# Performance work log

Measured on AMD Instinct MI355X. Metric: run time of the kernel, lower is better.

The kernel has to match this reference:

```python
import jax, jax.numpy as jnp
import numpy as np

N_HEADS = 8
D_KV = 64
NUM_BUCKETS = 32
MAX_DISTANCE = 128


def _relative_position_bucket(relative_position, bidirectional=True,
                              num_buckets=NUM_BUCKETS, max_distance=MAX_DISTANCE):
    # Faithful port of T5Attention._relative_position_bucket (bidirectional path).
    n = -relative_position
    if bidirectional:
        num_buckets //= 2
        ret = (n < 0).astype(jnp.int32) * num_buckets
        n = jnp.abs(n)
    else:
        ret = jnp.zeros_like(n)
        n = jnp.maximum(n, 0)
    max_exact = num_buckets // 2
    is_small = n < max_exact
    val_if_large = max_exact + (
        jnp.log(n.astype(jnp.float32) / max_exact)
        / np.log(max_distance / max_exact)
        * (num_buckets - max_exact)
    ).astype(jnp.int32)
    val_if_large = jnp.minimum(val_if_large, num_buckets - 1)
    return ret + jnp.where(is_small, n, val_if_large)


def setup_inputs() -> dict:
    key = jax.random.key(0)
    ks = jax.random.split(key, 6)
    bs, qlen, d_model = 2, 2048, 512
    inner = N_HEADS * D_KV
    s = 1.0 / np.sqrt(d_model)
    return {
        "input": jax.random.normal(ks[0], (bs, qlen, d_model), jnp.float32),
        "Wq": jax.random.normal(ks[1], (d_model, inner), jnp.float32) * s,
        "Wk": jax.random.normal(ks[2], (d_model, inner), jnp.float32) * s,
        "Wv": jax.random.normal(ks[3], (d_model, inner), jnp.float32) * s,
        "Wo": jax.random.normal(ks[4], (inner, d_model), jnp.float32) * s,
        "rel_bias": jax.random.normal(ks[5], (NUM_BUCKETS, N_HEADS), jnp.float32),
    }


def reference(input, Wq, Wk, Wv, Wo, rel_bias):
    bs, qlen, d_model = input.shape

    def shape(x):  # [b, s, inner] -> [b, h, s, d]
        return x.reshape(bs, qlen, N_HEADS, D_KV).transpose(0, 2, 1, 3)

    q = shape(input @ Wq)
    k = shape(input @ Wk)
    v = shape(input @ Wv)

    # Raw scores (T5: no 1/sqrt(d) scaling)
    scores = jnp.einsum("bhqd,bhkd->bhqk", q, k)

    # Relative position bias: bucket [q, k] -> [h, q, k]
    pos = jnp.arange(qlen)
    rel_pos = pos[None, :] - pos[:, None]  # memory - query
    buckets = _relative_position_bucket(rel_pos, bidirectional=True)
    position_bias = rel_bias[buckets].transpose(2, 0, 1)[None]  # [1, h, q, k]

    scores = scores + position_bias
    weights = jax.nn.softmax(scores.astype(jnp.float32), axis=-1).astype(scores.dtype)

    context = jnp.einsum("bhqk,bhkd->bhqd", weights, v)
    context = context.transpose(0, 2, 1, 3).reshape(bs, qlen, N_HEADS * D_KV)
    return context @ Wo
```

## Files before the change

### kernel.cpp

```cpp
#include <hip/hip_runtime.h>
#include <hip/hip_bf16.h>
#include <cmath>

typedef __bf16 bf16_t;
typedef __bf16 bf16x8 __attribute__((ext_vector_type(8)));
typedef __bf16 bf16x4 __attribute__((ext_vector_type(4)));
typedef float f32x4 __attribute__((ext_vector_type(4)));

#define QLEN 2048
#define DMODEL 512
#define NH 8
#define DKV 64
#define INNER 512
#define LOG2E 1.44269504f
#define THR_LOG2 11.5415603f

__global__ __launch_bounds__(256) void cvt_split(const float* __restrict__ in,
                                                 bf16_t* __restrict__ hi,
                                                 bf16_t* __restrict__ lo, int n4) {
  int i = blockIdx.x * 256 + threadIdx.x;
  if (i >= n4) return;
  float4 v = reinterpret_cast<const float4*>(in)[i];
  bf16x4 h, l;
  #pragma unroll
  for (int j = 0; j < 4; ++j) {
    float x = (&v.x)[j];
    bf16_t hb = (bf16_t)x;
    h[j] = hb;
    l[j] = (bf16_t)(x - (float)hb);
  }
  reinterpret_cast<bf16x4*>(hi)[i] = h;
  reinterpret_cast<bf16x4*>(lo)[i] = l;
}

__global__ __launch_bounds__(256) void transpose512_split_all(
    const float* __restrict__ W0, const float* __restrict__ W1,
    const float* __restrict__ W2, const float* __restrict__ W3,
    bf16_t* __restrict__ H0, bf16_t* __restrict__ L0,
    bf16_t* __restrict__ H1, bf16_t* __restrict__ L1,
    bf16_t* __restrict__ H2, bf16_t* __restrict__ L2,
    bf16_t* __restrict__ H3, bf16_t* __restrict__ L3) {
  __shared__ float tile[32][33];
  int z = blockIdx.z;
  const float* W = z == 0 ? W0 : z == 1 ? W1 : z == 2 ? W2 : W3;
  bf16_t* Whi    = z == 0 ? H0 : z == 1 ? H1 : z == 2 ? H2 : H3;
  bf16_t* Wlo    = z == 0 ? L0 : z == 1 ? L1 : z == 2 ? L2 : L3;
  int bk = blockIdx.x * 32, bn = blockIdx.y * 32;
  int tx = threadIdx.x, ty = threadIdx.y;
  #pragma unroll
  for (int i = 0; i < 32; i += 8)
    tile[ty + i][tx] = W[(size_t)(bk + ty + i) * DMODEL + bn + tx];
  __syncthreads();
  #pragma unroll
  for (int i = 0; i < 32; i += 8) {
    float v = tile[tx][ty + i];
    bf16_t hb = (bf16_t)v;
    size_t o = (size_t)(bn + ty + i) * DMODEL + bk + tx;
    Whi[o] = hb;
    Wlo[o] = (bf16_t)(v - (float)hb);
  }
}

template<int MODE>
__global__ __launch_bounds__(256) void gemm64(const bf16_t* __restrict__ A,
                                              const bf16_t* __restrict__ Bt,
                                              bf16_t* __restrict__ Cb,
                                              float* __restrict__ Cf) {
  __shared__ bf16_t sA[64 * 72];
  __shared__ bf16_t sB[64 * 72];
  const int m0 = blockIdx.x * 64, n0 = blockIdx.y * 64;
  const int tid = threadIdx.x;
  const int lane = tid & 63, w = tid >> 6;
  const int wr = (w >> 1) * 32, wc = (w & 1) * 32;
  const int l16 = lane & 15, lg = lane >> 4;

  f32x4 acc[2][2] = {};

  for (int k0 = 0; k0 < DMODEL; k0 += 64) {
    #pragma unroll
    for (int i = 0; i < 2; ++i) {
      int chunk = tid + i * 256;
      int row = chunk >> 3, c8 = (chunk & 7) * 8;
      *reinterpret_cast<bf16x8*>(&sA[row * 72 + c8]) =
          *reinterpret_cast<const bf16x8*>(&A[(size_t)(m0 + row) * DMODEL + k0 + c8]);
      *reinterpret_cast<bf16x8*>(&sB[row * 72 + c8]) =
          *reinterpret_cast<const bf16x8*>(&Bt[(size_t)(n0 + row) * DMODEL + k0 + c8]);
    }
    __syncthreads();
    #pragma unroll
    for (int ks = 0; ks < 2; ++ks) {
      bf16x8 af[2], bfr[2];
      #pragma unroll
      for (int i = 0; i < 2; ++i)
        af[i] = *reinterpret_cast<const bf16x8*>(&sA[(wr + i * 16 + l16) * 72 + ks * 32 + lg * 8]);
      #pragma unroll
      for (int j = 0; j < 2; ++j)
        bfr[j] = *reinterpret_cast<const bf16x8*>(&sB[(wc + j * 16 + l16) * 72 + ks * 32 + lg * 8]);
      #pragma unroll
      for (int i = 0; i < 2; ++i)
        #pragma unroll
        for (int j = 0; j < 2; ++j)
          acc[i][j] = __builtin_amdgcn_mfma_f32_16x16x32_bf16(af[i], bfr[j], acc[i][j], 0, 0, 0);
    }
    __syncthreads();
  }

  #pragma unroll
  for (int i = 0; i < 2; ++i)
    #pragma unroll
    for (int j = 0; j < 2; ++j)
      #pragma unroll
      for (int r = 0; r < 4; ++r) {
        int m = m0 + wr + i * 16 + lg * 4 + r;
        int n = n0 + wc + j * 16 + l16;
        float v = acc[i][j][r];
        if (MODE == 1) {
          int b = m >> 11, s = m & (QLEN - 1);
          Cb[(size_t)(b * INNER + n) * QLEN + s] = (bf16_t)v;
        } else {
          Cf[(size_t)m * DMODEL + n] = v;
        }
      }
}

__global__ __launch_bounds__(256) void gemm_qk_split(const bf16_t* __restrict__ Ah,
                                                     const bf16_t* __restrict__ Al,
                                                     const bf16_t* __restrict__ Bqh,
                                                     const bf16_t* __restrict__ Bql,
                                                     const bf16_t* __restrict__ Bkh,
                                                     const bf16_t* __restrict__ Bkl,
                                                     bf16_t* __restrict__ Qh,
                                                     bf16_t* __restrict__ Ql,
                                                     bf16_t* __restrict__ Kh,
                                                     bf16_t* __restrict__ Kl) {
  __shared__ bf16_t sAh[64 * 72];
  __shared__ bf16_t sAl[64 * 72];
  __shared__ bf16_t sBh[128 * 72];
  __shared__ bf16_t sBl[128 * 72];
  const int m0 = blockIdx.x * 64;
  const int n0g = blockIdx.y * 128;
  const bool isK = n0g >= 512;
  const int n0 = n0g & 511;
  const bf16_t* __restrict__ Bh = isK ? Bkh : Bqh;
  const bf16_t* __restrict__ Bl = isK ? Bkl : Bql;
  bf16_t* __restrict__ Ch = isK ? Kh : Qh;
  bf16_t* __restrict__ Cl = isK ? Kl : Ql;

  const int tid = threadIdx.x;
  const int lane = tid & 63, w = tid >> 6;
  const int wr = (w >> 1) * 32, wc = (w & 1) * 64;
  const int l16 = lane & 15, lg = lane >> 4;

  f32x4 acc[2][4] = {};

  for (int k0 = 0; k0 < DMODEL; k0 += 64) {
    #pragma unroll
    for (int i = 0; i < 2; ++i) {
      int chunk = tid + i * 256;
      int row = chunk >> 3, c8 = (chunk & 7) * 8;
      size_t ga = (size_t)(m0 + row) * DMODEL + k0 + c8;
      *reinterpret_cast<bf16x8*>(&sAh[row * 72 + c8]) = *reinterpret_cast<const bf16x8*>(&Ah[ga]);
      *reinterpret_cast<bf16x8*>(&sAl[row * 72 + c8]) = *reinterpret_cast<const bf16x8*>(&Al[ga]);
    }
    #pragma unroll
    for (int i = 0; i < 4; ++i) {
      int chunk = tid + i * 256;
      int row = chunk >> 3, c8 = (chunk & 7) * 8;
      size_t gb = (size_t)(n0 + row) * DMODEL + k0 + c8;
      *reinterpret_cast<bf16x8*>(&sBh[row * 72 + c8]) = *reinterpret_cast<const bf16x8*>(&Bh[gb]);
      *reinterpret_cast<bf16x8*>(&sBl[row * 72 + c8]) = *reinterpret_cast<const bf16x8*>(&Bl[gb]);
    }
    __syncthreads();
    #pragma unroll
    for (int ks = 0; ks < 2; ++ks) {
      bf16x8 ah[2], al[2], bh[4], bl[4];
      #pragma unroll
      for (int i = 0; i < 2; ++i) {
        int ro = (wr + i * 16 + l16) * 72 + ks * 32 + lg * 8;
        ah[i] = *reinterpret_cast<const bf16x8*>(&sAh[ro]);
        al[i] = *reinterpret_cast<const bf16x8*>(&sAl[ro]);
      }
      #pragma unroll
      for (int j = 0; j < 4; ++j) {
        int ro = (wc + j * 16 + l16) * 72 + ks * 32 + lg * 8;
        bh[j] = *reinterpret_cast<const bf16x8*>(&sBh[ro]);
        bl[j] = *reinterpret_cast<const bf16x8*>(&sBl[ro]);
      }
      #pragma unroll
      for (int i = 0; i < 2; ++i)
        #pragma unroll
        for (int j = 0; j < 4; ++j) {
          acc[i][j] = __builtin_amdgcn_mfma_f32_16x16x32_bf16(ah[i], bh[j], acc[i][j], 0, 0, 0);
          acc[i][j] = __builtin_amdgcn_mfma_f32_16x16x32_bf16(ah[i], bl[j], acc[i][j], 0, 0, 0);
          acc[i][j] = __builtin_amdgcn_mfma_f32_16x16x32_bf16(al[i], bh[j], acc[i][j], 0, 0, 0);
        }
    }
    __syncthreads();
  }

  #pragma unroll
  for (int i = 0; i < 2; ++i)
    #pragma unroll
    for (int j = 0; j < 4; ++j)
      #pragma unroll
      for (int r = 0; r < 4; ++r) {
        int m = m0 + wr + i * 16 + lg * 4 + r;
        int n = n0 + wc + j * 16 + l16;
        float v = acc[i][j][r];
        if (!isK) v *= LOG2E;
        bf16_t hb = (bf16_t)v;
        size_t o = (size_t)m * INNER + n;
        Ch[o] = hb;
        if (!isK) Cl[o] = (bf16_t)(v - (float)hb);
      }
}

__device__ __forceinline__ float redmax16(float v) {
  v = fmaxf(v, __shfl_xor(v, 1));
  v = fmaxf(v, __shfl_xor(v, 2));
  v = fmaxf(v, __shfl_xor(v, 4));
  v = fmaxf(v, __shfl_xor(v, 8));
  return v;
}
__device__ __forceinline__ float redsum16(float v) {
  v += __shfl_xor(v, 1);
  v += __shfl_xor(v, 2);
  v += __shfl_xor(v, 4);
  v += __shfl_xor(v, 8);
  return v;
}
__device__ __forceinline__ int t5_bucket_abs(int n) {
  if (n < 8)  return n;
  if (n < 12) return 8;
  if (n < 16) return 9;
  if (n < 23) return 10;
  if (n < 32) return 11;
  if (n < 46) return 12;
  if (n < 64) return 13;
  if (n < 91) return 14;
  return 15;
}

#define SPS 68
#define SVS 136

struct StageRegs { bf16x8 kh[2], v[2]; };

__device__ __forceinline__ void stage_load(StageRegs& r, const bf16_t* __restrict__ Kh,
                                           const bf16_t* __restrict__ Vt,
                                           int b, int h, int k0, int tid) {
  #pragma unroll
  for (int i = 0; i < 2; ++i) {
    int chunk = tid + i * 512;
    int krow = chunk >> 3, kc8 = (chunk & 7) * 8;
    int vrow = chunk >> 4, vc8 = (chunk & 15) * 8;
    r.kh[i] = *reinterpret_cast<const bf16x8*>(
        &Kh[(size_t)(b * QLEN + k0 + krow) * INNER + h * DKV + kc8]);
    r.v[i] = *reinterpret_cast<const bf16x8*>(
        &Vt[(size_t)((b * NH + h) * DKV + vrow) * QLEN + k0 + vc8]);
  }
}
__device__ __forceinline__ void stage_write(const StageRegs& r, bf16_t* dKh, bf16_t* dV,
                                            int tid) {
  #pragma unroll
  for (int i = 0; i < 2; ++i) {
    int chunk = tid + i * 512;
    int krow = chunk >> 3, kc8 = (chunk & 7) * 8;
    int vrow = chunk >> 4, vc8 = (chunk & 15) * 8;
    *reinterpret_cast<bf16x8*>(&dKh[krow * 72 + kc8]) = r.kh[i];
    *reinterpret_cast<bf16x8*>(&dV [vrow * SVS + vc8]) = r.v[i];
  }
}

__global__ __launch_bounds__(512, 4) void attn_kernel(const bf16_t* __restrict__ Qh,
                                                      const bf16_t* __restrict__ Ql,
                                                      const bf16_t* __restrict__ Kh,
                                                      const bf16_t* __restrict__ Vt,
                                                      const float* __restrict__ relb,
                                                      bf16_t* __restrict__ ctx) {
  __shared__ bf16_t sKh[128 * 72];
  __shared__ bf16_t sV [64 * SVS];
  __shared__ bf16_t sP [2][64 * SPS];
  __shared__ float sM[2][64], sL[2][64];
  __shared__ float sBiasH[32];
  float* sAcc = (float*)&sP[0][0];

  const int id = blockIdx.x;
  const int lin = (id & 7) * 64 + (id >> 3);
  const int qt = lin & 31, h = (lin >> 5) & 7, b = lin >> 8;

  const int tid = threadIdx.x, lane = tid & 63, w = tid >> 6;
  const int l16 = lane & 15, lg = lane >> 4;
  const int q0 = qt * 64;
  const int qg = w & 3, half = w >> 2;
  const int wq = qg * 16;
  const int kh0 = half * 64;

  if (tid < 32) sBiasH[tid] = relb[tid * NH + h] * LOG2E;

  bf16x8 qh[2], ql[2];
  #pragma unroll
  for (int ks = 0; ks < 2; ++ks) {
    size_t o = (size_t)(b * QLEN + q0 + wq + l16) * INNER + h * DKV + ks * 32 + lg * 8;
    qh[ks] = *reinterpret_cast<const bf16x8*>(&Qh[o]);
    ql[ks] = *reinterpret_cast<const bf16x8*>(&Ql[o]);
  }

  f32x4 acc[4] = {};
  float mrow[4], lpart[4];
  #pragma unroll
  for (int r = 0; r < 4; ++r) { mrow[r] = -INFINITY; lpart[r] = 0.f; }

  const int NT = QLEN / 128;
  StageRegs sreg;
  stage_load(sreg, Kh, Vt, b, h, 0, tid);
  stage_write(sreg, sKh, sV, tid);
  __syncthreads();

  for (int kt = 0; kt < NT; ++kt) {
    const int k0 = kt * 128;
    const bool pf = (kt + 1 < NT);
    if (pf) stage_load(sreg, Kh, Vt, b, h, k0 + 128, tid);

    f32x4 s[4] = {};
    __builtin_amdgcn_s_setprio(1);
    #pragma unroll
    for (int ks = 0; ks < 2; ++ks) {
      bf16x8 kf[4];
      #pragma unroll
      for (int ni = 0; ni < 4; ++ni)
        kf[ni] = *reinterpret_cast<const bf16x8*>(
            &sKh[(kh0 + ni * 16 + l16) * 72 + ks * 32 + lg * 8]);
      #pragma unroll
      for (int ni = 0; ni < 4; ++ni) {
        s[ni] = __builtin_amdgcn_mfma_f32_16x16x32_bf16(qh[ks], kf[ni], s[ni], 0, 0, 0);
        s[ni] = __builtin_amdgcn_mfma_f32_16x16x32_bf16(ql[ks], kf[ni], s[ni], 0, 0, 0);
      }
    }
    __builtin_amdgcn_s_setprio(0);

    const int kbase = k0 + kh0;
    const int dmin = q0 - (kbase + 63);
    const int dmax = q0 + 63 - kbase;
    const bool farP = dmin >= 91, farN = dmax <= -91;
    float fbias = 0.f;
    if (farP) fbias = sBiasH[15];
    else if (farN) fbias = sBiasH[31];
    else {
      #pragma unroll
      for (int ni = 0; ni < 4; ++ni) {
        int kcol = kbase + ni * 16 + l16;
        #pragma unroll
        for (int r = 0; r < 4; ++r) {
          int qrow = q0 + wq + lg * 4 + r;
          int d = qrow - kcol;
          int n = d < 0 ? -d : d;
          int bk = t5_bucket_abs(n) + (d < 0 ? 16 : 0);
          s[ni][r] += sBiasH[bk];
        }
      }
    }

    float c[4], tmx[4];
    #pragma unroll
    for (int r = 0; r < 4; ++r) {
      tmx[r] = fmaxf(fmaxf(s[0][r], s[1][r]), fmaxf(s[2][r], s[3][r]));
      c[r] = mrow[r] - fbias;
    }
    float u = fmaxf(fmaxf(tmx[0] - c[0], tmx[1] - c[1]), fmaxf(tmx[2] - c[2], tmx[3] - c[3]));
    if (__any(u > THR_LOG2)) {
      #pragma unroll
      for (int r = 0; r < 4; ++r) {
        float rm = redmax16(tmx[r]) + fbias;
        float mnew = fmaxf(mrow[r], rm);
        float alpha = exp2f(mrow[r] - mnew);
        mrow[r] = mnew;
        c[r] = mnew - fbias;
        lpart[r] *= alpha;
        #pragma unroll
        for (int di = 0; di < 4; ++di) acc[di][r] *= alpha;
      }
    }

    #pragma unroll
    for (int r = 0; r < 4; ++r) {
      float ps = 0.f;
      #pragma unroll
      for (int ni = 0; ni < 4; ++ni) {
        float p = exp2f(s[ni][r] - c[r]);
        ps += p;
        sP[half][(wq + lg * 4 + r) * SPS + ni * 16 + l16] = (bf16_t)p;
      }
      lpart[r] += ps;
    }

    __builtin_amdgcn_s_setprio(1);
    #pragma unroll
    for (int ks = 0; ks < 2; ++ks) {
      bf16x8 pfr, vf[4];
      pfr = *reinterpret_cast<const bf16x8*>(&sP[half][(wq + l16) * SPS + ks * 32 + lg * 8]);
      #pragma unroll
      for (int di = 0; di < 4; ++di)
        vf[di] = *reinterpret_cast<const bf16x8*>(
            &sV[(di * 16 + l16) * SVS + kh0 + ks * 32 + lg * 8]);
      #pragma unroll
      for (int di = 0; di < 4; ++di)
        acc[di] = __builtin_amdgcn_mfma_f32_16x16x32_bf16(pfr, vf[di], acc[di], 0, 0, 0);
    }
    __builtin_amdgcn_s_setprio(0);

    __syncthreads();
    if (pf) stage_write(sreg, sKh, sV, tid);
    __syncthreads();
  }

  float lrow[4];
  #pragma unroll
  for (int r = 0; r < 4; ++r) lrow[r] = redsum16(lpart[r]);

  if (l16 == 0) {
    #pragma unroll
    for (int r = 0; r < 4; ++r) {
      int row = wq + lg * 4 + r;
      sM[half][row] = mrow[r];
      sL[half][row] = lrow[r];
    }
  }
  __syncthreads();

  float eh[4], denom[4];
  #pragma unroll
  for (int r = 0; r < 4; ++r) {
    int row = wq + lg * 4 + r;
    float m0 = sM[0][row], m1 = sM[1][row];
    float l0 = sL[0][row], l1 = sL[1][row];
    float M = fmaxf(m0, m1);
    float e0 = exp2f(m0 - M), e1 = exp2f(m1 - M);
    denom[r] = l0 * e0 + l1 * e1;
    eh[r] = half ? e1 : e0;
  }

  if (half == 1) {
    #pragma unroll
    for (int di = 0; di < 4; ++di)
      #pragma unroll
      for (int r = 0; r < 4; ++r)
        sAcc[(wq + lg * 4 + r) * SPS + di * 16 + l16] = acc[di][r] * eh[r];
  }
  __syncthreads();

  if (half == 0) {
    #pragma unroll
    for (int di = 0; di < 4; ++di)
      #pragma unroll
      for (int r = 0; r < 4; ++r) {
        int row = wq + lg * 4 + r;
        float v = (acc[di][r] * eh[r] + sAcc[row * SPS + di * 16 + l16]) / denom[r];
        ctx[(size_t)(b * QLEN + q0 + row) * INNER + h * DKV + di * 16 + l16] = (bf16_t)v;
      }
  }
}

extern "C" void kernel_launch(void* const* d_in, const int* in_sizes, int n_in,
                              void* d_out, int out_size, void* d_ws, size_t ws_size,
                              hipStream_t stream) {
  const float* X    = (const float*)d_in[0];
  const float* Wq   = (const float*)d_in[1];
  const float* Wk   = (const float*)d_in[2];
  const float* Wv   = (const float*)d_in[3];
  const float* Wo   = (const float*)d_in[4];
  const float* relb = (const float*)d_in[5];
  float* out = (float*)d_out;

  const size_t WSZ = 262144, XSZ = 2097152;
  bf16_t* ws   = (bf16_t*)d_ws;
  bf16_t* Wq_h = ws;              bf16_t* Wq_l = Wq_h + WSZ;
  bf16_t* Wk_h = Wq_l + WSZ;      bf16_t* Wk_l = Wk_h + WSZ;
  bf16_t* Wv_h = Wk_l + WSZ;      bf16_t* Wv_l = Wv_h + WSZ;
  bf16_t* Wo_h = Wv_l + WSZ;      bf16_t* Wo_l = Wo_h + WSZ;
  bf16_t* Xh   = Wo_l + WSZ;      bf16_t* Xl   = Xh + XSZ;
  bf16_t* Q_h  = Xl + XSZ;        bf16_t* Q_l  = Q_h + XSZ;
  bf16_t* K_h  = Q_l + XSZ;       bf16_t* K_l  = K_h + XSZ;
  bf16_t* Vt   = Xl;
  bf16_t* ctx  = Xh;

  transpose512_split_all<<<dim3(16, 16, 4), dim3(32, 8), 0, stream>>>(
      Wq, Wk, Wv, Wo, Wq_h, Wq_l, Wk_h, Wk_l, Wv_h, Wv_l, Wo_h, Wo_l);

  int n4 = (2 * QLEN * DMODEL) / 4;
  cvt_split<<<n4 / 256, 256, 0, stream>>>(X, Xh, Xl, n4);

  gemm_qk_split<<<dim3(64, 8), 256, 0, stream>>>(Xh, Xl, Wq_h, Wq_l, Wk_h, Wk_l,
                                                 Q_h, Q_l, K_h, K_l);
  gemm64<1><<<dim3(64, 8), 256, 0, stream>>>(Xh, Wv_h, Vt, nullptr);

  attn_kernel<<<dim3(512), 512, 0, stream>>>(Q_h, Q_l, K_h, Vt, relb, ctx);

  gemm64<2><<<dim3(64, 8), 256, 0, stream>>>(ctx, Wo_h, nullptr, out);
}
```

Before: 109.4 us.

## Split attention over key halves with a merge kernel and direct global K/V loads

The attention kernel now splits the key dimension into two halves, launching twice as many blocks. Each block writes a partial normalized context plus the row max and denominator to scratch space (reusing the output and weight buffers). A new merge kernel combines the two halves into ctx. K and V fragments are now read straight from global memory instead of being staged through shared memory with barriers, which cuts LDS use and allows higher occupancy (launch bounds 512,8). The cost is an extra kernel launch, extra global traffic for partials, and uncoalesced or L2-dependent K/V reads.

```diff
diff --git a/kernel.cpp b/kernel.cpp
--- a/kernel.cpp
+++ b/kernel.cpp
@@ -242,61 +242,33 @@
 }
 
 #define SPS 68
-#define SVS 136
-
-struct StageRegs { bf16x8 kh[2], v[2]; };
-
-__device__ __forceinline__ void stage_load(StageRegs& r, const bf16_t* __restrict__ Kh,
-                                           const bf16_t* __restrict__ Vt,
-                                           int b, int h, int k0, int tid) {
-  #pragma unroll
-  for (int i = 0; i < 2; ++i) {
-    int chunk = tid + i * 512;
-    int krow = chunk >> 3, kc8 = (chunk & 7) * 8;
-    int vrow = chunk >> 4, vc8 = (chunk & 15) * 8;
-    r.kh[i] = *reinterpret_cast<const bf16x8*>(
-        &Kh[(size_t)(b * QLEN + k0 + krow) * INNER + h * DKV + kc8]);
-    r.v[i] = *reinterpret_cast<const bf16x8*>(
-        &Vt[(size_t)((b * NH + h) * DKV + vrow) * QLEN + k0 + vc8]);
-  }
-}
-__device__ __forceinline__ void stage_write(const StageRegs& r, bf16_t* dKh, bf16_t* dV,
-                                            int tid) {
-  #pragma unroll
-  for (int i = 0; i < 2; ++i) {
-    int chunk = tid + i * 512;
-    int krow = chunk >> 3, kc8 = (chunk & 7) * 8;
-    int vrow = chunk >> 4, vc8 = (chunk & 15) * 8;
-    *reinterpret_cast<bf16x8*>(&dKh[krow * 72 + kc8]) = r.kh[i];
-    *reinterpret_cast<bf16x8*>(&dV [vrow * SVS + vc8]) = r.v[i];
-  }
-}
-
-__global__ __launch_bounds__(512, 4) void attn_kernel(const bf16_t* __restrict__ Qh,
+#define HALFELEMS 2097152
+
+__global__ __launch_bounds__(512, 8) void attn_kernel(const bf16_t* __restrict__ Qh,
                                                       const bf16_t* __restrict__ Ql,
                                                       const bf16_t* __restrict__ Kh,
                                                       const bf16_t* __restrict__ Vt,
                                                       const float* __restrict__ relb,
-                                                      bf16_t* __restrict__ ctx) {
-  __shared__ bf16_t sKh[128 * 72];
-  __shared__ bf16_t sV [64 * SVS];
-  __shared__ bf16_t sP [2][64 * SPS];
+                                                      bf16_t* __restrict__ pPart,
+                                                      float* __restrict__ pMl) {
+  __shared__ bf16_t sP[2][64 * SPS];
   __shared__ float sM[2][64], sL[2][64];
   __shared__ float sBiasH[32];
   float* sAcc = (float*)&sP[0][0];
 
   const int id = blockIdx.x;
-  const int lin = (id & 7) * 64 + (id >> 3);
-  const int qt = lin & 31, h = (lin >> 5) & 7, b = lin >> 8;
+  const int lin = (id & 7) * 128 + (id >> 3);
+  const int qt = lin & 31, h = (lin >> 5) & 7, b = (lin >> 8) & 1, sp = lin >> 9;
 
   const int tid = threadIdx.x, lane = tid & 63, w = tid >> 6;
   const int l16 = lane & 15, lg = lane >> 4;
   const int q0 = qt * 64;
   const int qg = w & 3, half = w >> 2;
   const int wq = qg * 16;
-  const int kh0 = half * 64;
+  const int kw0 = sp * 1024 + half * 512;
 
   if (tid < 32) sBiasH[tid] = relb[tid * NH + h] * LOG2E;
+  __syncthreads();
 
   bf16x8 qh[2], ql[2];
   #pragma unroll
@@ -311,16 +283,13 @@
   #pragma unroll
   for (int r = 0; r < 4; ++r) { mrow[r] = -INFINITY; lpart[r] = 0.f; }
 
-  const int NT = QLEN / 128;
-  StageRegs sreg;
-  stage_load(sreg, Kh, Vt, b, h, 0, tid);
-  stage_write(sreg, sKh, sV, tid);
-  __syncthreads();
-
-  for (int kt = 0; kt < NT; ++kt) {
-    const int k0 = kt * 128;
-    const bool pf = (kt + 1 < NT);
-    if (pf) stage_load(sreg, Kh, Vt, b, h, k0 + 128, tid);
+  const size_t kLane = (size_t)l16 * INNER + lg * 8;
+  const size_t vLane = (size_t)l16 * QLEN + lg * 8;
+  size_t kBase = (size_t)(b * QLEN + kw0) * INNER + h * DKV;
+  size_t vBase = (size_t)((b * NH + h) * DKV) * QLEN + kw0;
+
+  for (int it = 0; it < 8; ++it) {
+    const int kbase = kw0 + it * 64;
 
     f32x4 s[4] = {};
     __builtin_amdgcn_s_setprio(1);
@@ -330,7 +299,7 @@
       #pragma unroll
       for (int ni = 0; ni < 4; ++ni)
         kf[ni] = *reinterpret_cast<const bf16x8*>(
-            &sKh[(kh0 + ni * 16 + l16) * 72 + ks * 32 + lg * 8]);
+            &Kh[kBase + (size_t)ni * 16 * INNER + kLane + ks * 32]);
       #pragma unroll
       for (int ni = 0; ni < 4; ++ni) {
         s[ni] = __builtin_amdgcn_mfma_f32_16x16x32_bf16(qh[ks], kf[ni], s[ni], 0, 0, 0);
@@ -339,7 +308,6 @@
     }
     __builtin_amdgcn_s_setprio(0);
 
-    const int kbase = k0 + kh0;
     const int dmin = q0 - (kbase + 63);
     const int dmax = q0 + 63 - kbase;
     const bool farP = dmin >= 91, farN = dmax <= -91;
@@ -402,16 +370,15 @@
       #pragma unroll
       for (int di = 0; di < 4; ++di)
         vf[di] = *reinterpret_cast<const bf16x8*>(
-            &sV[(di * 16 + l16) * SVS + kh0 + ks * 32 + lg * 8]);
+            &Vt[vBase + (size_t)di * 16 * QLEN + vLane + ks * 32]);
       #pragma unroll
       for (int di = 0; di < 4; ++di)
         acc[di] = __builtin_amdgcn_mfma_f32_16x16x32_bf16(pfr, vf[di], acc[di], 0, 0, 0);
     }
     __builtin_amdgcn_s_setprio(0);
 
-    __syncthreads();
-    if (pf) stage_write(sreg, sKh, sV, tid);
-    __syncthreads();
+    kBase += (size_t)64 * INNER;
+    vBase += 64;
   }
 
   float lrow[4];
@@ -428,7 +395,7 @@
   }
   __syncthreads();
 
-  float eh[4], denom[4];
+  float eh[4], denom[4], Mc[4];
   #pragma unroll
   for (int r = 0; r < 4; ++r) {
     int row = wq + lg * 4 + r;
@@ -438,6 +405,7 @@
     float e0 = exp2f(m0 - M), e1 = exp2f(m1 - M);
     denom[r] = l0 * e0 + l1 * e1;
     eh[r] = half ? e1 : e0;
+    Mc[r] = M;
   }
 
   if (half == 1) {
@@ -450,15 +418,46 @@
   __syncthreads();
 
   if (half == 0) {
+    const int rowbase = (b * NH + h) * QLEN + q0 + wq;
     #pragma unroll
     for (int di = 0; di < 4; ++di)
       #pragma unroll
       for (int r = 0; r < 4; ++r) {
-        int row = wq + lg * 4 + r;
-        float v = (acc[di][r] * eh[r] + sAcc[row * SPS + di * 16 + l16]) / denom[r];
-        ctx[(size_t)(b * QLEN + q0 + row) * INNER + h * DKV + di * 16 + l16] = (bf16_t)v;
-      }
-  }
+        int rl = wq + lg * 4 + r;
+        float v = (acc[di][r] * eh[r] + sAcc[rl * SPS + di * 16 + l16]) / denom[r];
+        pPart[(size_t)sp * HALFELEMS + (size_t)(rowbase + lg * 4 + r) * 64 + di * 16 + l16] =
+            (bf16_t)v;
+      }
+    if (l16 == 0) {
+      #pragma unroll
+      for (int r = 0; r < 4; ++r) {
+        int row = rowbase + lg * 4 + r;
+        float2 v; v.x = Mc[r]; v.y = denom[r];
+        *reinterpret_cast<float2*>(&pMl[sp * 65536 + row * 2]) = v;
+      }
+    }
+  }
+}
+
+__global__ __launch_bounds__(256) void attn_merge(const bf16_t* __restrict__ pPart,
+                                                  const float* __restrict__ pMl,
+                                                  bf16_t* __restrict__ ctx) {
+  int idx = blockIdx.x * 256 + threadIdx.x;
+  int row = idx >> 3, d8 = (idx & 7) * 8;
+  bf16x8 p0 = *reinterpret_cast<const bf16x8*>(&pPart[(size_t)row * 64 + d8]);
+  bf16x8 p1 = *reinterpret_cast<const bf16x8*>(&pPart[HALFELEMS + (size_t)row * 64 + d8]);
+  float2 ml0 = *reinterpret_cast<const float2*>(&pMl[row * 2]);
+  float2 ml1 = *reinterpret_cast<const float2*>(&pMl[65536 + row * 2]);
+  float M = fmaxf(ml0.x, ml1.x);
+  float w0 = ml0.y * exp2f(ml0.x - M), w1 = ml1.y * exp2f(ml1.x - M);
+  float inv = 1.f / (w0 + w1);
+  w0 *= inv; w1 *= inv;
+  int b = row >> 14, h = (row >> 11) & 7, q = row & 2047;
+  bf16x8 o;
+  #pragma unroll
+  for (int j = 0; j < 8; ++j)
+    o[j] = (bf16_t)((float)p0[j] * w0 + (float)p1[j] * w1);
+  *reinterpret_cast<bf16x8*>(&ctx[((size_t)(b * QLEN + q)) * INNER + h * DKV + d8]) = o;
 }
 
 extern "C" void kernel_launch(void* const* d_in, const int* in_sizes, int n_in,
@@ -483,6 +482,8 @@
   bf16_t* K_h  = Q_l + XSZ;       bf16_t* K_l  = K_h + XSZ;
   bf16_t* Vt   = Xl;
   bf16_t* ctx  = Xh;
+  bf16_t* pPart = (bf16_t*)d_out;
+  float*  pMl   = (float*)Wq_h;
 
   transpose512_split_all<<<dim3(16, 16, 4), dim3(32, 8), 0, stream>>>(
       Wq, Wk, Wv, Wo, Wq_h, Wq_l, Wk_h, Wk_l, Wv_h, Wv_l, Wo_h, Wo_l);
@@ -494,7 +495,8 @@
                                                  Q_h, Q_l, K_h, K_l);
   gemm64<1><<<dim3(64, 8), 256, 0, stream>>>(Xh, Wv_h, Vt, nullptr);
 
-  attn_kernel<<<dim3(512), 512, 0, stream>>>(Q_h, Q_l, K_h, Vt, relb, ctx);
+  attn_kernel<<<dim3(1024), 512, 0, stream>>>(Q_h, Q_l, K_h, Vt, relb, pPart, pMl);
+  attn_merge<<<dim3(1024), 256, 0, stream>>>(pPart, pMl, ctx);
 
   gemm64<2><<<dim3(64, 8), 256, 0, stream>>>(ctx, Wo_h, nullptr, out);
 }
```

Measured after the change: 250.0 us. 2.29x slower.
